# Kernel tuning notes

Hardware: AMD Instinct MI355X
Metric: run time of the kernel (lower is better)

The kernel has to match this reference:

```python
import jax, jax.numpy as jnp
import numpy as np

# Device / mapping constants from the source (is_low_resistance=True branch)
V_REF = 0.25
G_MIN = 0.1
G_MAX = 1.0
K_V = 2.0 * V_REF  # x_to_V scale
N_AVG = 2.18
N_STD = 0.115


def setup_inputs() -> dict:
    key = jax.random.key(0)
    k_x, k_wp, k_wn, k_n = jax.random.split(key, 4)
    n_in, n_out, batch = 1024, 512, 128
    stdv = 1.0 / np.sqrt(n_in)
    x = jax.random.uniform(k_x, (batch, n_in), dtype=jnp.float32)
    w_pos = 0.5 + stdv * jax.random.normal(k_wp, (n_in, n_out), dtype=jnp.float32)
    w_neg = 0.5 + stdv * jax.random.normal(k_wn, (n_in, n_out), dtype=jnp.float32)
    b_pos = 0.5 * jnp.ones((n_out,), jnp.float32)
    b_neg = 0.5 * jnp.ones((n_out,), jnp.float32)
    # per-device I-V nonlinearity parameter n ~ N(n_avg, n_std), one per crossbar cell
    n_param = N_AVG + N_STD * jax.random.normal(k_n, (n_in + 1, 2 * n_out), dtype=jnp.float32)
    return {"x": x, "w_pos": w_pos, "w_neg": w_neg, "b_pos": b_pos, "b_neg": b_neg,
            "n_param": n_param}


def _memristor_dense(x, w_pos, w_neg, b_pos, b_neg, n_param):
    x = jnp.clip(x, 0.0, 1.0)
    # append bias rows, interleave pos/neg along output axis -> (n_in+1, 2*n_out)
    cw_pos = jnp.concatenate([w_pos, b_pos[None, :]], axis=0)
    cw_neg = jnp.concatenate([w_neg, b_neg[None, :]], axis=0)
    w = jnp.stack([cw_pos, cw_neg], axis=-1).reshape(cw_pos.shape[0], -1)
    # append ones column to inputs (bias voltage line)
    inp = jnp.concatenate([x, jnp.ones((x.shape[0], 1), x.dtype)], axis=1)  # (B, n_in+1)
    # weight -> effective conductance (differential scheme), then offset by G_min
    max_w = jnp.max(jnp.abs(w))
    k_G = (G_MAX - G_MIN) / max_w
    G = jnp.abs(k_G * w) + G_MIN  # (n_in+1, 2*n_out)
    # input -> voltage
    V = K_V * inp  # (B, n_in+1)
    # nonlinear-parameter I-V model: I = sign(V) * G * V_ref * (|V|/V_ref) ** (log2(n) + 1)
    # (satisfies n = I(2*V_ref) / (2 * I(V_ref)))
    exponent = jnp.log2(n_param) + 1.0  # (n_in+1, 2*n_out)
    v_ratio = jnp.abs(V) / V_REF  # (B, n_in+1)
    vr = v_ratio[:, :, None]  # (B, n_in+1, 1)
    vr_safe = jnp.where(vr > 0, vr, 1.0)
    pow_term = jnp.where(vr > 0, vr_safe ** exponent[None, :, :], 0.0)  # (B, n_in+1, 2*n_out)
    I_ind = jnp.sign(V)[:, :, None] * (G * V_REF)[None, :, :] * pow_term
    # sum currents along bit lines
    I = jnp.sum(I_ind, axis=1)  # (B, 2*n_out)
    # currents -> outputs (differential pairs are interleaved)
    y = (I[:, 0::2] - I[:, 1::2]) / (K_V * k_G)  # (B, n_out)
    return y


def reference(x, w_pos, w_neg, b_pos, b_neg, n_param):
    return _memristor_dense(x, w_pos, w_neg, b_pos, b_neg, n_param)
```

## Files before the change

### kernel.cpp

```cpp
#include <hip/hip_runtime.h>
#include <hip/hip_bf16.h>


#define LOG2F(v)  __builtin_amdgcn_logf(v)
#define EXP2F(v)  __builtin_amdgcn_exp2f(v)

#define NJ 16
#define NB 16
#define KI 64
#define KROW4 65
#define LROW 68

#define NPART 32

__global__ __launch_bounds__(256) void setup_kernel(
    const float* __restrict__ w_pos, const float* __restrict__ w_neg,
    const float* __restrict__ b_pos, const float* __restrict__ b_neg,
    float* __restrict__ y, float* __restrict__ ws) {
  const int t = threadIdx.x, blk = blockIdx.x;
  float4 z4 = make_float4(0.f, 0.f, 0.f, 0.f);
  float4* y4 = (float4*)y;
  y4[blk * 512 + t]       = z4;
  y4[blk * 512 + 256 + t] = z4;
  const float4* wp4 = (const float4*)w_pos;
  const float4* wn4 = (const float4*)w_neg;
  float m = 0.0f;
  #pragma unroll 4
  for (int r = 0; r < 16; ++r) {
    int i = blk * 4096 + r * 256 + t;
    float4 a = wp4[i], b = wn4[i];
    m = fmaxf(m, fmaxf(fmaxf(fabsf(a.x), fabsf(a.y)), fmaxf(fabsf(a.z), fabsf(a.w))));
    m = fmaxf(m, fmaxf(fmaxf(fabsf(b.x), fabsf(b.y)), fmaxf(fabsf(b.z), fabsf(b.w))));
  }
  if (blk == 0) {
    m = fmaxf(m, fmaxf(fabsf(b_pos[t]), fabsf(b_pos[t + 256])));
    m = fmaxf(m, fmaxf(fabsf(b_neg[t]), fabsf(b_neg[t + 256])));
  }
  #pragma unroll
  for (int off = 32; off > 0; off >>= 1)
    m = fmaxf(m, __shfl_down(m, off, 64));
  __shared__ float sm[4];
  int lane = t & 63, wv = t >> 6;
  if (lane == 0) sm[wv] = m;
  __syncthreads();
  if (t == 0)
    ws[blk] = fmaxf(fmaxf(sm[0], sm[1]), fmaxf(sm[2], sm[3]));
}

__global__ __launch_bounds__(256) void memristor_kernel(
    const float* __restrict__ x, const float* __restrict__ w_pos,
    const float* __restrict__ w_neg, const float* __restrict__ b_pos,
    const float* __restrict__ b_neg, const float* __restrict__ n_param,
    const float* __restrict__ ws, float* __restrict__ y) {
  __shared__ float4 sP[NJ * KROW4];
  __shared__ float  sL[NB * LROW];

  float mw = 0.0f;
  #pragma unroll
  for (int i = 0; i < NPART; ++i) mw = fmaxf(mw, ws[i]);
  const float c0 = mw * (0.05f / 0.9f);

  const int j0 = blockIdx.x * NJ;
  const int b0 = blockIdx.y * NB;
  const int zt = blockIdx.z;
  const int t  = threadIdx.x;
  const int jj = t & 15;
  const int bb = t >> 4;
  float accP = 0.0f, accN = 0.0f;

  const float2* np2 = (const float2*)n_param;

  for (int c = 0; c < 4; ++c) {
    const int i0 = zt * 256 + c * KI;
    #pragma unroll
    for (int r = 0; r < (NB * KI) / 256; ++r) {
      int idx = r * 256 + t;
      int k  = idx & (KI - 1);
      int bl = idx >> 6;
      float v = x[(b0 + bl) * 1024 + i0 + k];
      v = fminf(fmaxf(v, 0.0f), 1.0f);
      sL[bl * LROW + k] = LOG2F(2.0f * v);
    }
    #pragma unroll
    for (int r = 0; r < (NJ * KI) / 256; ++r) {
      int idx = r * 256 + t;
      int jl = idx & (NJ - 1);
      int il = idx >> 4;
      int gi = i0 + il;
      float wp = w_pos[gi * 512 + j0 + jl];
      float wn = w_neg[gi * 512 + j0 + jl];
      float2 np = np2[gi * 512 + j0 + jl];
      sP[jl * KROW4 + il] = make_float4(
          fmaf(0.5f, fabsf(wp), c0), LOG2F(np.x) + 1.0f,
          fmaf(0.5f, fabsf(wn), c0), LOG2F(np.y) + 1.0f);
    }
    __syncthreads();
    const float4* pP = &sP[jj * KROW4];
    const float*  pL = &sL[bb * LROW];
    #pragma unroll 8
    for (int k = 0; k < KI; ++k) {
      float4 p = pP[k];
      float l  = pL[k];
      accP = fmaf(p.x, EXP2F(p.y * l), accP);
      accN = fmaf(p.z, EXP2F(p.w * l), accN);
    }
    __syncthreads();
  }

  if (zt == 3) {
    int jg = j0 + jj;
    float2 np = np2[1024 * 512 + jg];
    float a0 = fmaf(0.5f, fabsf(b_pos[jg]), c0);
    float a1 = fmaf(0.5f, fabsf(b_neg[jg]), c0);
    accP = fmaf(a0, EXP2F(LOG2F(np.x) + 1.0f), accP);
    accN = fmaf(a1, EXP2F(LOG2F(np.y) + 1.0f), accN);
  }

  atomicAdd(&y[(b0 + bb) * 512 + (j0 + jj)], accP - accN);
}

extern "C" void kernel_launch(void* const* d_in, const int* in_sizes, int n_in,
                              void* d_out, int out_size, void* d_ws, size_t ws_size,
                              hipStream_t stream) {
  const float* x       = (const float*)d_in[0];
  const float* w_pos   = (const float*)d_in[1];
  const float* w_neg   = (const float*)d_in[2];
  const float* b_pos   = (const float*)d_in[3];
  const float* b_neg   = (const float*)d_in[4];
  const float* n_param = (const float*)d_in[5];
  float* y   = (float*)d_out;
  float* wsf = (float*)d_ws;

  setup_kernel<<<dim3(NPART), dim3(256), 0, stream>>>(
      w_pos, w_neg, b_pos, b_neg, y, wsf);

  memristor_kernel<<<dim3(32, 8, 4), dim3(256), 0, stream>>>(
      x, w_pos, w_neg, b_pos, b_neg, n_param, wsf, y);
}
```

Before: 93.82 us.

## Precompute conductance/exponent table and input logs in a separate pass

Adds a second setup kernel that computes the per-cell conductance and log2(n)+1 exponent once into a packed float4 workspace table, and log2 of the clipped inputs into another workspace array. The main kernel then loads these precomputed values instead of recomputing logs for every batch tile. Previously each of the 8 batch-tile blocks redid the log2 of n_param for the same cells. The cost is an extra launch and an extra round trip of about 8 MB through global memory for the table.

Measured after the change: 95.91 us. 1.02x slower.

```diff
diff --git a/kernel.cpp b/kernel.cpp
--- a/kernel.cpp
+++ b/kernel.cpp
@@ -12,16 +12,15 @@
 #define LROW 68
 
 #define NPART 32
+#define T_OFF_B   256
+#define L_OFF_B   (T_OFF_B + 525824 * 16)
+#define NROW_T    1025
 
-__global__ __launch_bounds__(256) void setup_kernel(
+__global__ __launch_bounds__(256) void setup1_kernel(
     const float* __restrict__ w_pos, const float* __restrict__ w_neg,
     const float* __restrict__ b_pos, const float* __restrict__ b_neg,
-    float* __restrict__ y, float* __restrict__ ws) {
+    float* __restrict__ ws) {
   const int t = threadIdx.x, blk = blockIdx.x;
-  float4 z4 = make_float4(0.f, 0.f, 0.f, 0.f);
-  float4* y4 = (float4*)y;
-  y4[blk * 512 + t]       = z4;
-  y4[blk * 512 + 256 + t] = z4;
   const float4* wp4 = (const float4*)w_pos;
   const float4* wn4 = (const float4*)w_neg;
   float m = 0.0f;
@@ -47,18 +46,53 @@
     ws[blk] = fmaxf(fmaxf(sm[0], sm[1]), fmaxf(sm[2], sm[3]));
 }
 
-__global__ __launch_bounds__(256) void memristor_kernel(
+__global__ __launch_bounds__(256) void setup2_kernel(
     const float* __restrict__ x, const float* __restrict__ w_pos,
     const float* __restrict__ w_neg, const float* __restrict__ b_pos,
     const float* __restrict__ b_neg, const float* __restrict__ n_param,
-    const float* __restrict__ ws, float* __restrict__ y) {
-  __shared__ float4 sP[NJ * KROW4];
-  __shared__ float  sL[NB * LROW];
-
+    float* __restrict__ y, float* __restrict__ ws) {
+  const int t = threadIdx.x, blk = blockIdx.x;
   float mw = 0.0f;
   #pragma unroll
   for (int i = 0; i < NPART; ++i) mw = fmaxf(mw, ws[i]);
   const float c0 = mw * (0.05f / 0.9f);
+
+  if (blk < NROW_T) {
+    const int i = blk;
+    const float2* np2 = (const float2*)n_param;
+    float4* T4 = (float4*)((char*)ws + T_OFF_B);
+    #pragma unroll
+    for (int h = 0; h < 2; ++h) {
+      int j = t + h * 256;
+      float wp, wn;
+      if (i < 1024) { wp = w_pos[i * 512 + j]; wn = w_neg[i * 512 + j]; }
+      else          { wp = b_pos[j];           wn = b_neg[j]; }
+      float2 np = np2[i * 512 + j];
+      T4[i * 512 + j] = make_float4(
+          fmaf(0.5f, fabsf(wp), c0), LOG2F(np.x) + 1.0f,
+          fmaf(0.5f, fabsf(wn), c0), LOG2F(np.y) + 1.0f);
+    }
+    if (blk < 256) y[blk * 256 + t] = 0.0f;
+  } else {
+    const int b = blk - NROW_T;
+    float* L = (float*)((char*)ws + L_OFF_B);
+    #pragma unroll
+    for (int h = 0; h < 4; ++h) {
+      int i = t + h * 256;
+      float v = x[b * 1024 + i];
+      v = fminf(fmaxf(v, 0.0f), 1.0f);
+      L[b * 1024 + i] = LOG2F(2.0f * v);
+    }
+  }
+}
+
+__global__ __launch_bounds__(256) void memristor_kernel(
+    const float* __restrict__ ws_c, float* __restrict__ y) {
+  __shared__ float4 sP[NJ * KROW4];
+  __shared__ float  sL[NB * LROW];
+
+  const float4* T4 = (const float4*)((const char*)ws_c + T_OFF_B);
+  const float*  L  = (const float*)((const char*)ws_c + L_OFF_B);
 
   const int j0 = blockIdx.x * NJ;
   const int b0 = blockIdx.y * NB;
@@ -68,31 +102,19 @@
   const int bb = t >> 4;
   float accP = 0.0f, accN = 0.0f;
 
-  const float2* np2 = (const float2*)n_param;
-
   for (int c = 0; c < 4; ++c) {
     const int i0 = zt * 256 + c * KI;
-    #pragma unroll
-    for (int r = 0; r < (NB * KI) / 256; ++r) {
-      int idx = r * 256 + t;
-      int k  = idx & (KI - 1);
-      int bl = idx >> 6;
-      float v = x[(b0 + bl) * 1024 + i0 + k];
-      v = fminf(fmaxf(v, 0.0f), 1.0f);
-      sL[bl * LROW + k] = LOG2F(2.0f * v);
+    {
+      int bl = t >> 4, k4 = t & 15;
+      float4 v = *(const float4*)&L[(b0 + bl) * 1024 + i0 + k4 * 4];
+      *(float4*)&sL[bl * LROW + k4 * 4] = v;
     }
     #pragma unroll
     for (int r = 0; r < (NJ * KI) / 256; ++r) {
       int idx = r * 256 + t;
       int jl = idx & (NJ - 1);
       int il = idx >> 4;
-      int gi = i0 + il;
-      float wp = w_pos[gi * 512 + j0 + jl];
-      float wn = w_neg[gi * 512 + j0 + jl];
-      float2 np = np2[gi * 512 + j0 + jl];
-      sP[jl * KROW4 + il] = make_float4(
-          fmaf(0.5f, fabsf(wp), c0), LOG2F(np.x) + 1.0f,
-          fmaf(0.5f, fabsf(wn), c0), LOG2F(np.y) + 1.0f);
+      sP[jl * KROW4 + il] = T4[(i0 + il) * 512 + j0 + jl];
     }
     __syncthreads();
     const float4* pP = &sP[jj * KROW4];
@@ -108,12 +130,9 @@
   }
 
   if (zt == 3) {
-    int jg = j0 + jj;
-    float2 np = np2[1024 * 512 + jg];
-    float a0 = fmaf(0.5f, fabsf(b_pos[jg]), c0);
-    float a1 = fmaf(0.5f, fabsf(b_neg[jg]), c0);
-    accP = fmaf(a0, EXP2F(LOG2F(np.x) + 1.0f), accP);
-    accN = fmaf(a1, EXP2F(LOG2F(np.y) + 1.0f), accN);
+    float4 p = T4[1024 * 512 + j0 + jj];
+    accP = fmaf(p.x, EXP2F(p.y), accP);
+    accN = fmaf(p.z, EXP2F(p.w), accN);
   }
 
   atomicAdd(&y[(b0 + bb) * 512 + (j0 + jj)], accP - accN);
@@ -131,9 +150,11 @@
   float* y   = (float*)d_out;
   float* wsf = (float*)d_ws;
 
-  setup_kernel<<<dim3(NPART), dim3(256), 0, stream>>>(
-      w_pos, w_neg, b_pos, b_neg, y, wsf);
+  setup1_kernel<<<dim3(NPART), dim3(256), 0, stream>>>(
+      w_pos, w_neg, b_pos, b_neg, wsf);
 
-  memristor_kernel<<<dim3(32, 8, 4), dim3(256), 0, stream>>>(
-      x, w_pos, w_neg, b_pos, b_neg, n_param, wsf, y);
+  setup2_kernel<<<dim3(NROW_T + 128), dim3(256), 0, stream>>>(
+      x, w_pos, w_neg, b_pos, b_neg, n_param, y, wsf);
+
+  memristor_kernel<<<dim3(32, 8, 4), dim3(256), 0, stream>>>(wsf, y);
 }
```
